# Kernel tuning notes

Hardware: AMD Instinct MI355X
Metric: run time of the kernel (lower is better)

The kernel has to match this reference:

```python
import jax, jax.numpy as jnp
import numpy as np

N_NODES = 100000
N_EDGES = 1600000
D_IN = 128
D_OUT = 128


def setup_inputs() -> dict:
    key = jax.random.key(0)
    k = jax.random.split(key, 7)
    x = jax.random.normal(k[0], (N_NODES, D_IN), dtype=jnp.float32)
    edge_index = jax.random.randint(k[1], (2, N_EDGES), 0, N_NODES, dtype=jnp.int32)
    # MLP params (PyTorch Linear-style scaling)
    s1 = 1.0 / np.sqrt(D_IN)
    s2 = 1.0 / np.sqrt(D_OUT)
    W1 = jax.random.uniform(k[2], (D_IN, D_OUT), jnp.float32, -s1, s1)
    b1 = jax.random.uniform(k[3], (D_OUT,), jnp.float32, -s1, s1)
    W2 = jax.random.uniform(k[4], (D_OUT, D_OUT), jnp.float32, -s2, s2)
    b2 = jax.random.uniform(k[5], (D_OUT,), jnp.float32, -s2, s2)
    eps = jnp.zeros((), dtype=jnp.float32)  # train_eps=True, init 0
    return {"x": x, "edge_index": edge_index, "W1": W1, "b1": b1, "W2": W2, "b2": b2, "eps": eps}


def reference(x, edge_index, W1, b1, W2, b2, eps):
    src, dst = edge_index[0], edge_index[1]  # flow: source_to_target
    # scatter-add neighbor aggregation: agg[i] = sum_{(j->i)} x[j]
    agg = jax.ops.segment_sum(x[src], dst, num_segments=x.shape[0])  # [N, D_IN]
    h = (1.0 + eps) * x + agg
    # 2-layer MLP: Linear -> ReLU -> Linear
    h = jax.nn.relu(h @ W1 + b1)
    return h @ W2 + b2
```

## Files before the change

### kernel.cpp

```cpp
#include <hip/hip_runtime.h>

#define NN    100000
#define NE    1600000
#define DD    128
#define CAP   48
#define NBKT  391
#define PCAP  4608
#define EPB   4096
#define NCVT  12500

typedef float  f4v __attribute__((ext_vector_type(4)));
typedef float  f2v __attribute__((ext_vector_type(2)));
typedef short  s8v __attribute__((ext_vector_type(8)));
typedef unsigned short u16;
typedef unsigned int   u32;

static __device__ __forceinline__ u16 f2bf(float f) {
    u32 u = __float_as_uint(f);
    return (u16)((u + 0x7fffu + ((u >> 16) & 1u)) >> 16);
}
static __device__ __forceinline__ f2v unpk(u32 p) {
    f2v r;
    r.x = __uint_as_float(p << 16);
    r.y = __uint_as_float(p & 0xffff0000u);
    return r;
}

static __device__ __forceinline__ void cvt_rows(
    const float* __restrict__ x, u32* __restrict__ xbp, int row_base, int tid)
{
    const int row  = row_base + (tid >> 6);
    const int lane = tid & 63;
    const float* xp = x + (size_t)row * DD;
    xbp[(size_t)row * 64 + lane] =
        (u32)f2bf(xp[lane]) | ((u32)f2bf(xp[lane + 64]) << 16);
}

__global__ __launch_bounds__(256) void part_conv(
    const float* __restrict__ x, const int* __restrict__ ei,
    u32* __restrict__ xbp, u32* __restrict__ pairs, int* __restrict__ gcnt)
{
    __shared__ int hist[NBKT];
    __shared__ int base[NBKT];
    const int b   = blockIdx.x;
    const int tid = threadIdx.x;
    if (b >= NBKT) {
        cvt_rows(x, xbp, (b - NBKT) * 4, tid);
        return;
    }
    const int e0 = b * EPB;

    int sv[16], dv[16];
#pragma unroll
    for (int t = 0; t < 16; ++t) {
        const int e = e0 + t * 256 + tid;
        if (e < NE) { sv[t] = ei[e]; dv[t] = ei[NE + e]; }
        else        { dv[t] = -1; sv[t] = 0; }
    }

    for (int i = tid; i < NBKT; i += 256) hist[i] = 0;
    __syncthreads();

#pragma unroll
    for (int t = 0; t < 16; ++t)
        if (dv[t] >= 0) atomicAdd(&hist[dv[t] >> 8], 1);
    __syncthreads();

    for (int i = tid; i < NBKT; i += 256) {
        const int h = hist[i];
        base[i] = h ? atomicAdd(&gcnt[i * 16], h) : 0;
        hist[i] = 0;
    }
    __syncthreads();

#pragma unroll
    for (int t = 0; t < 16; ++t)
        if (dv[t] >= 0) {
            const int bk = dv[t] >> 8;
            const int r  = base[bk] + atomicAdd(&hist[bk], 1);
            if (r < PCAP)
                pairs[(size_t)bk * PCAP + r] = ((u32)sv[t] << 8) | (u32)(dv[t] & 255);
        }
}

__global__ __launch_bounds__(256) void build_conv(
    const float* __restrict__ x,
    const float* __restrict__ W1, const float* __restrict__ W2,
    const u32* __restrict__ pairs, const int* __restrict__ gcnt,
    u32* __restrict__ xbp, u16* __restrict__ img1, u16* __restrict__ img2,
    int* __restrict__ cnt, int* __restrict__ eidx)
{
    __shared__ int cl[256], cur[256];
    const int b   = blockIdx.x;
    const int tid = threadIdx.x;

    if (b >= NBKT) {
        if (b < NBKT + NCVT) {
            cvt_rows(x, xbp, 50000 + (b - NBKT) * 4, tid);
        } else if (b < NBKT + NCVT + 8) {
            const int gid  = (b - NBKT - NCVT) * 256 + tid;
            const int frag = gid >> 6;
            const int lane = gid & 63;
            const int n  = (frag >> 2) * 16 + (lane & 15);
            const int k0 = (frag & 3) * 32 + (lane >> 4) * 8;
            u16* o1 = img1 + (size_t)gid * 8;
            u16* o2 = img2 + (size_t)gid * 8;
#pragma unroll
            for (int j = 0; j < 8; ++j) {
                o1[j] = f2bf(W1[(size_t)(k0 + j) * DD + n]);
                o2[j] = f2bf(W2[(size_t)(k0 + j) * DD + n]);
            }
        } else {
            if (tid < 64) xbp[(size_t)NN * 64 + tid] = 0;
        }
        return;
    }

    const int n   = min(gcnt[b * 16], PCAP);
    const u32* pp = pairs + (size_t)b * PCAP;

    u32 pv[18];
#pragma unroll
    for (int t = 0; t < 18; ++t) {
        const int i = t * 256 + tid;
        if (i < n) pv[t] = pp[i];
    }

    cl[tid] = 0; cur[tid] = 0;
    __syncthreads();

#pragma unroll
    for (int t = 0; t < 18; ++t) {
        const int i = t * 256 + tid;
        if (i < n) atomicAdd(&cl[pv[t] & 255], 1);
    }
    __syncthreads();

    const int g = b * 256 + tid;
    if (g < NN) cnt[g] = cl[tid];

#pragma unroll
    for (int t = 0; t < 18; ++t) {
        const int i = t * 256 + tid;
        if (i < n) {
            const u32 p  = pv[t];
            const int ld = p & 255;
            const int r  = atomicAdd(&cur[ld], 1);
            if (r < CAP) eidx[(size_t)(b * 256 + ld) * CAP + r] = (int)(p >> 8);
        }
    }
}

__global__ __launch_bounds__(256, 8) void gather_kernel(
    const u32* __restrict__ xbp, const int* __restrict__ cnt,
    const int* __restrict__ eidx, const float* __restrict__ epsp,
    u16* __restrict__ hb)
{
    const int node  = blockIdx.x * 4 + (threadIdx.x >> 6);
    const int lane  = threadIdx.x & 63;
    const int noded = __builtin_amdgcn_readfirstlane(node);

    const u32   ps = xbp[((size_t)noded << 6) + lane];
    const float sc = 1.0f + epsp[0];

    const int deg = __builtin_amdgcn_readfirstlane(min(cnt[noded], CAP));
    int idxv = NN;
    if (lane < deg) idxv = eidx[(size_t)noded * CAP + lane];

    f2v acc[4] = {};
    u32 p[32];
    const int nb = (deg + 15) >> 4;

    if (nb > 0) {
#pragma unroll
        for (int t = 0; t < 16; ++t) {
            const u32 s = (u32)__builtin_amdgcn_readlane(idxv, t);
            p[t] = xbp[((size_t)s << 6) + lane];
        }
    }
    if (nb > 1) {
#pragma unroll
        for (int t = 0; t < 16; ++t) {
            const u32 s = (u32)__builtin_amdgcn_readlane(idxv, 16 + t);
            p[16 + t] = xbp[((size_t)s << 6) + lane];
        }
    }
    if (nb > 0) {
#pragma unroll
        for (int t = 0; t < 16; ++t) acc[t & 3] += unpk(p[t]);
    }
    if (nb > 1) {
#pragma unroll
        for (int t = 0; t < 16; ++t) acc[t & 3] += unpk(p[16 + t]);
    }
    if (nb > 2) {
#pragma unroll
        for (int t = 0; t < 16; ++t) {
            const u32 s = (u32)__builtin_amdgcn_readlane(idxv, 32 + t);
            p[t] = xbp[((size_t)s << 6) + lane];
        }
#pragma unroll
        for (int t = 0; t < 16; ++t) acc[t & 3] += unpk(p[t]);
    }

    const f2v s01 = acc[0] + acc[1];
    const f2v s23 = acc[2] + acc[3];
    const f2v st  = s01 + s23;
    const f2v sv  = unpk(ps);
    hb[(size_t)noded * DD + lane]      = f2bf(fmaf(sc, sv.x, st.x));
    hb[(size_t)noded * DD + lane + 64] = f2bf(fmaf(sc, sv.y, st.y));
}

__global__ __launch_bounds__(256) void mlp_kernel(
    const u16* __restrict__ hb,
    const u16* __restrict__ img1, const u16* __restrict__ img2,
    const float* __restrict__ b1, const float* __restrict__ b2,
    float* __restrict__ out)
{
    __shared__ char lds_raw[4 * 8448];
    const int tid  = threadIdx.x;
    const int wave = tid >> 6;
    const int lane = tid & 63;
    const int l15  = lane & 15;
    const int quad = lane >> 4;

    float* fstage = (float*)(lds_raw + wave * 8448);
    u16*   hstage = (u16*)fstage;

    int rbase = (blockIdx.x * 4 + wave) * 16;
    if (rbase > NN - 16) rbase = NN - 16;

    float bv1[8], bv2[8];
#pragma unroll
    for (int nt = 0; nt < 8; ++nt) {
        bv1[nt] = b1[nt * 16 + l15];
        bv2[nt] = b2[nt * 16 + l15];
    }

    s8v afrag[4];
#pragma unroll
    for (int kc = 0; kc < 4; ++kc)
        afrag[kc] = *(const s8v*)(hb + (size_t)(rbase + l15) * DD + kc * 32 + quad * 8);

    f4v acc1[8] = {};
#pragma unroll
    for (int kc = 0; kc < 4; ++kc)
#pragma unroll
        for (int nt = 0; nt < 8; ++nt) {
            const s8v bfr = *(const s8v*)(img1 + ((size_t)((nt * 4 + kc) * 64 + lane)) * 8);
            acc1[nt] = __builtin_amdgcn_mfma_f32_16x16x32_bf16(afrag[kc], bfr, acc1[nt], 0, 0, 0);
        }

#pragma unroll
    for (int nt = 0; nt < 8; ++nt)
#pragma unroll
        for (int r = 0; r < 4; ++r) {
            const float v = fmaxf(acc1[nt][r] + bv1[nt], 0.0f);
            hstage[(quad * 4 + r) * 136 + nt * 16 + l15] = f2bf(v);
        }
    __syncthreads();

    s8v a2[4];
#pragma unroll
    for (int kc = 0; kc < 4; ++kc)
        a2[kc] = *(const s8v*)&hstage[l15 * 136 + kc * 32 + quad * 8];

    f4v acc2[8] = {};
#pragma unroll
    for (int kc = 0; kc < 4; ++kc)
#pragma unroll
        for (int nt = 0; nt < 8; ++nt) {
            const s8v bfr = *(const s8v*)(img2 + ((size_t)((nt * 4 + kc) * 64 + lane)) * 8);
            acc2[nt] = __builtin_amdgcn_mfma_f32_16x16x32_bf16(a2[kc], bfr, acc2[nt], 0, 0, 0);
        }

    __syncthreads();
#pragma unroll
    for (int nt = 0; nt < 8; ++nt)
#pragma unroll
        for (int r = 0; r < 4; ++r)
            fstage[(quad * 4 + r) * 132 + nt * 16 + l15] = acc2[nt][r] + bv2[nt];
    __syncthreads();

#pragma unroll
    for (int i = 0; i < 8; ++i) {
        const int m  = (lane >> 5) + 2 * i;
        const int c4 = lane & 31;
        const f4v v = *(const f4v*)&fstage[m * 132 + c4 * 4];
        *(f4v*)(out + (size_t)(rbase + m) * DD + c4 * 4) = v;
    }
}

extern "C" void kernel_launch(void* const* d_in, const int* in_sizes, int n_in,
                              void* d_out, int out_size, void* d_ws, size_t ws_size,
                              hipStream_t stream) {
    const float* x   = (const float*)d_in[0];
    const int*   ei  = (const int*)d_in[1];
    const float* W1  = (const float*)d_in[2];
    const float* b1  = (const float*)d_in[3];
    const float* W2  = (const float*)d_in[4];
    const float* b2  = (const float*)d_in[5];
    const float* eps = (const float*)d_in[6];
    float* out = (float*)d_out;

    u32* xbp   = (u32*)d_ws;
    u16* hb    = (u16*)(xbp + (size_t)(NN + 1) * 64);
    int* eidx  = (int*)(hb + (size_t)NN * DD);
    int* cnt   = eidx + (size_t)NN * CAP;
    u16* img1  = (u16*)(cnt + NN);
    u16* img2  = img1 + (size_t)DD * DD;
    u32* pairs = (u32*)(img2 + (size_t)DD * DD);
    int* gcnt  = (int*)(pairs + (size_t)NBKT * PCAP);

    hipMemsetAsync(gcnt, 0, (size_t)NBKT * 16 * sizeof(int), stream);
    part_conv    <<<NBKT + NCVT,        256, 0, stream>>>(x, ei, xbp, pairs, gcnt);
    build_conv   <<<NBKT + NCVT + 9,    256, 0, stream>>>(x, W1, W2, pairs, gcnt,
                                                          xbp, img1, img2, cnt, eidx);
    gather_kernel<<<NN / 4,             256, 0, stream>>>(xbp, cnt, eidx, eps, hb);
    mlp_kernel   <<<(NN / 16 + 3) / 4,  256, 0, stream>>>(hb, img1, img2, b1, b2, out);
}
```

Before: 226.2 us.

## Fuse neighbor gather into MLP kernel via swizzled LDS row staging

Merges the gather kernel and the MLP kernel so each wave aggregates 16 nodes sequentially and writes the bf16 rows into swizzled shared memory, which then feed the MFMA layers directly. This removes the global round-trip of the intermediate bf16 h buffer and one kernel launch. In exchange, gather parallelism per wave drops: one wave now walks 16 nodes serially instead of one node per wave. Occupancy is also capped by the larger LDS footprint and the launch bound of 3, which could reduce memory-latency hiding for the random gathers.

```diff
diff --git a/kernel.cpp b/kernel.cpp
--- a/kernel.cpp
+++ b/kernel.cpp
@@ -151,84 +151,25 @@
     }
 }
 
-__global__ __launch_bounds__(256, 8) void gather_kernel(
+__global__ __launch_bounds__(256, 3) void gather_mlp(
     const u32* __restrict__ xbp, const int* __restrict__ cnt,
     const int* __restrict__ eidx, const float* __restrict__ epsp,
-    u16* __restrict__ hb)
-{
-    const int node  = blockIdx.x * 4 + (threadIdx.x >> 6);
-    const int lane  = threadIdx.x & 63;
-    const int noded = __builtin_amdgcn_readfirstlane(node);
-
-    const u32   ps = xbp[((size_t)noded << 6) + lane];
-    const float sc = 1.0f + epsp[0];
-
-    const int deg = __builtin_amdgcn_readfirstlane(min(cnt[noded], CAP));
-    int idxv = NN;
-    if (lane < deg) idxv = eidx[(size_t)noded * CAP + lane];
-
-    f2v acc[4] = {};
-    u32 p[32];
-    const int nb = (deg + 15) >> 4;
-
-    if (nb > 0) {
-#pragma unroll
-        for (int t = 0; t < 16; ++t) {
-            const u32 s = (u32)__builtin_amdgcn_readlane(idxv, t);
-            p[t] = xbp[((size_t)s << 6) + lane];
-        }
-    }
-    if (nb > 1) {
-#pragma unroll
-        for (int t = 0; t < 16; ++t) {
-            const u32 s = (u32)__builtin_amdgcn_readlane(idxv, 16 + t);
-            p[16 + t] = xbp[((size_t)s << 6) + lane];
-        }
-    }
-    if (nb > 0) {
-#pragma unroll
-        for (int t = 0; t < 16; ++t) acc[t & 3] += unpk(p[t]);
-    }
-    if (nb > 1) {
-#pragma unroll
-        for (int t = 0; t < 16; ++t) acc[t & 3] += unpk(p[16 + t]);
-    }
-    if (nb > 2) {
-#pragma unroll
-        for (int t = 0; t < 16; ++t) {
-            const u32 s = (u32)__builtin_amdgcn_readlane(idxv, 32 + t);
-            p[t] = xbp[((size_t)s << 6) + lane];
-        }
-#pragma unroll
-        for (int t = 0; t < 16; ++t) acc[t & 3] += unpk(p[t]);
-    }
-
-    const f2v s01 = acc[0] + acc[1];
-    const f2v s23 = acc[2] + acc[3];
-    const f2v st  = s01 + s23;
-    const f2v sv  = unpk(ps);
-    hb[(size_t)noded * DD + lane]      = f2bf(fmaf(sc, sv.x, st.x));
-    hb[(size_t)noded * DD + lane + 64] = f2bf(fmaf(sc, sv.y, st.y));
-}
-
-__global__ __launch_bounds__(256) void mlp_kernel(
-    const u16* __restrict__ hb,
     const u16* __restrict__ img1, const u16* __restrict__ img2,
     const float* __restrict__ b1, const float* __restrict__ b2,
     float* __restrict__ out)
 {
+    __shared__ char rows[64 * 256];
     __shared__ char lds_raw[4 * 8448];
+
     const int tid  = threadIdx.x;
     const int wave = tid >> 6;
     const int lane = tid & 63;
     const int l15  = lane & 15;
     const int quad = lane >> 4;
 
-    float* fstage = (float*)(lds_raw + wave * 8448);
-    u16*   hstage = (u16*)fstage;
-
-    int rbase = (blockIdx.x * 4 + wave) * 16;
-    if (rbase > NN - 16) rbase = NN - 16;
+    const int rb = blockIdx.x * 64 + wave * 16;
+
+    const float sc = 1.0f + epsp[0];
 
     float bv1[8], bv2[8];
 #pragma unroll
@@ -237,10 +178,63 @@
         bv2[nt] = b2[nt * 16 + l15];
     }
 
+    int cv = 0;
+    {
+        int nd = rb + l15; if (nd > NN - 1) nd = NN - 1;
+        if (lane < 16) cv = cnt[nd];
+    }
+
+    int idx[16];
+#pragma unroll
+    for (int n = 0; n < 16; ++n) {
+        int nd = rb + n; if (nd > NN - 1) nd = NN - 1;
+        const int dgc = min(__builtin_amdgcn_readlane(cv, n), CAP);
+        const int v   = eidx[(size_t)nd * CAP + lane];
+        idx[n] = (lane < dgc) ? v : NN;
+    }
+
+#pragma unroll
+    for (int n = 0; n < 16; ++n) {
+        int nd = rb + n; if (nd > NN - 1) nd = NN - 1;
+        const int dgc = min(__builtin_amdgcn_readlane(cv, n), CAP);
+        const u32 ps  = xbp[((size_t)nd << 6) + lane];
+        const int nb  = (dgc + 15) >> 4;
+
+        f2v a0 = {0.f, 0.f}, a1 = {0.f, 0.f}, a2 = {0.f, 0.f}, a3 = {0.f, 0.f};
+        for (int bb = 0; bb < nb; ++bb) {
+            u32 p[16];
+#pragma unroll
+            for (int t = 0; t < 16; ++t) {
+                const u32 s = (u32)__builtin_amdgcn_readlane(idx[n], bb * 16 + t);
+                p[t] = xbp[((size_t)s << 6) + lane];
+            }
+#pragma unroll
+            for (int t = 0; t < 16; t += 4) {
+                a0 += unpk(p[t]); a1 += unpk(p[t + 1]);
+                a2 += unpk(p[t + 2]); a3 += unpk(p[t + 3]);
+            }
+        }
+        const f2v st = (a0 + a1) + (a2 + a3);
+        const f2v sv = unpk(ps);
+        const u16 r0 = f2bf(fmaf(sc, sv.x, st.x));
+        const u16 r1 = f2bf(fmaf(sc, sv.y, st.y));
+
+        char* rp = rows + (wave * 16 + n) * 256;
+        const int swz = (n & 7) << 4;
+        *(u16*)(rp + ((lane * 2) ^ swz))       = r0;
+        *(u16*)(rp + ((128 + lane * 2) ^ swz)) = r1;
+    }
+    __syncthreads();
+
+    float* fstage = (float*)(lds_raw + wave * 8448);
+    u16*   hstage = (u16*)fstage;
+
     s8v afrag[4];
 #pragma unroll
-    for (int kc = 0; kc < 4; ++kc)
-        afrag[kc] = *(const s8v*)(hb + (size_t)(rbase + l15) * DD + kc * 32 + quad * 8);
+    for (int kc = 0; kc < 4; ++kc) {
+        const int boff = (kc * 64 + quad * 16) ^ ((l15 & 7) << 4);
+        afrag[kc] = *(const s8v*)(rows + (wave * 16 + l15) * 256 + boff);
+    }
 
     f4v acc1[8] = {};
 #pragma unroll
@@ -260,10 +254,10 @@
         }
     __syncthreads();
 
-    s8v a2[4];
+    s8v a2f[4];
 #pragma unroll
     for (int kc = 0; kc < 4; ++kc)
-        a2[kc] = *(const s8v*)&hstage[l15 * 136 + kc * 32 + quad * 8];
+        a2f[kc] = *(const s8v*)&hstage[l15 * 136 + kc * 32 + quad * 8];
 
     f4v acc2[8] = {};
 #pragma unroll
@@ -271,7 +265,7 @@
 #pragma unroll
         for (int nt = 0; nt < 8; ++nt) {
             const s8v bfr = *(const s8v*)(img2 + ((size_t)((nt * 4 + kc) * 64 + lane)) * 8);
-            acc2[nt] = __builtin_amdgcn_mfma_f32_16x16x32_bf16(a2[kc], bfr, acc2[nt], 0, 0, 0);
+            acc2[nt] = __builtin_amdgcn_mfma_f32_16x16x32_bf16(a2f[kc], bfr, acc2[nt], 0, 0, 0);
         }
 
     __syncthreads();
@@ -286,8 +280,10 @@
     for (int i = 0; i < 8; ++i) {
         const int m  = (lane >> 5) + 2 * i;
         const int c4 = lane & 31;
-        const f4v v = *(const f4v*)&fstage[m * 132 + c4 * 4];
-        *(f4v*)(out + (size_t)(rbase + m) * DD + c4 * 4) = v;
+        if (rb + m < NN) {
+            const f4v v = *(const f4v*)&fstage[m * 132 + c4 * 4];
+            *(f4v*)(out + (size_t)(rb + m) * DD + c4 * 4) = v;
+        }
     }
 }
 
@@ -304,18 +300,17 @@
     float* out = (float*)d_out;
 
     u32* xbp   = (u32*)d_ws;
-    u16* hb    = (u16*)(xbp + (size_t)(NN + 1) * 64);
-    int* eidx  = (int*)(hb + (size_t)NN * DD);
-    int* cnt   = eidx + (size_t)NN * CAP;
+    int* eidx  = (int*)(xbp + (size_t)(NN + 1) * 64);
+    int* cnt   = eidx + (size_t)NN * CAP + 64;
     u16* img1  = (u16*)(cnt + NN);
     u16* img2  = img1 + (size_t)DD * DD;
     u32* pairs = (u32*)(img2 + (size_t)DD * DD);
     int* gcnt  = (int*)(pairs + (size_t)NBKT * PCAP);
 
     hipMemsetAsync(gcnt, 0, (size_t)NBKT * 16 * sizeof(int), stream);
-    part_conv    <<<NBKT + NCVT,        256, 0, stream>>>(x, ei, xbp, pairs, gcnt);
-    build_conv   <<<NBKT + NCVT + 9,    256, 0, stream>>>(x, W1, W2, pairs, gcnt,
-                                                          xbp, img1, img2, cnt, eidx);
-    gather_kernel<<<NN / 4,             256, 0, stream>>>(xbp, cnt, eidx, eps, hb);
-    mlp_kernel   <<<(NN / 16 + 3) / 4,  256, 0, stream>>>(hb, img1, img2, b1, b2, out);
-}
+    part_conv <<<NBKT + NCVT,     256, 0, stream>>>(x, ei, xbp, pairs, gcnt);
+    build_conv<<<NBKT + NCVT + 9, 256, 0, stream>>>(x, W1, W2, pairs, gcnt,
+                                                    xbp, img1, img2, cnt, eidx);
+    gather_mlp<<<(NN + 63) / 64,  256, 0, stream>>>(xbp, cnt, eidx, eps,
+                                                    img1, img2, b1, b2, out);
+}
```

New measurement: 234.4 us. 1.04x slower.
